# Optimization experiments

Measured on AMD Instinct MI355X. Metric: run time of the kernel, lower is better.

Reference implementation:

```python
import jax, jax.numpy as jnp
import numpy as np

DIM = 256
HEADS = 8
HEAD_DIM = DIM // HEADS
HIDDEN = DIM * 4


def layer_norm(x, w, b, eps=1e-5):
    m = jnp.mean(x, axis=-1, keepdims=True)
    v = jnp.mean((x - m) ** 2, axis=-1, keepdims=True)
    return (x - m) / jnp.sqrt(v + eps) * w + b


def setup_inputs() -> dict:
    key = jax.random.key(0)
    ks = jax.random.split(key, 12)
    s = lambda fan_in: 1.0 / np.sqrt(fan_in)
    inp = {
        "x0": jax.random.normal(ks[0], (2, 32, 64, DIM), jnp.float32),
        "x1": jax.random.normal(ks[1], (2, 32, 64, DIM), jnp.float32),
        # torch Linear weights stored [out, in], no bias for qk/v/merge
        "qk_w": jax.random.uniform(ks[2], (DIM, DIM), jnp.float32, -s(DIM), s(DIM)),
        "v_w": jax.random.uniform(ks[3], (DIM, DIM), jnp.float32, -s(DIM), s(DIM)),
        "merge_w": jax.random.uniform(ks[4], (DIM, DIM), jnp.float32, -s(DIM), s(DIM)),
        "ln1_w": jnp.ones((DIM,), jnp.float32),
        "ln1_b": jnp.zeros((DIM,), jnp.float32),
        "ln2_w": jnp.ones((DIM,), jnp.float32),
        "ln2_b": jnp.zeros((DIM,), jnp.float32),
        "fc1_w": jax.random.uniform(ks[5], (HIDDEN, 2 * DIM), jnp.float32, -s(2 * DIM), s(2 * DIM)),
        "fc1_b": jnp.zeros((HIDDEN,), jnp.float32),
        "fc2_w": jax.random.uniform(ks[6], (DIM, HIDDEN), jnp.float32, -s(HIDDEN), s(HIDDEN)),
        "fc2_b": jnp.zeros((DIM,), jnp.float32),
        "gamma": jnp.ones((DIM,), jnp.float32),
    }
    return inp


def reference(x0, x1, qk_w, v_w, merge_w, ln1_w, ln1_b, ln2_w, ln2_b,
              fc1_w, fc1_b, fc2_w, fc2_b, gamma):
    N0, L0, WW0, C = x0.shape
    N1, L1, WW1, _ = x1.shape
    x0f = x0.reshape(N0, L0 * WW0, C)
    x1f = x1.reshape(N1, L1 * WW1, C)

    n0 = layer_norm(x0f, ln1_w, ln1_b)
    n1 = layer_norm(x1f, ln1_w, ln1_b)

    def heads(t):  # [N, S, C] -> [N, H, S, Dh]
        N, S, _ = t.shape
        return t.reshape(N, S, HEADS, HEAD_DIM).transpose(0, 2, 1, 3)

    scale = HEAD_DIM ** -0.25  # sqrt of softmax_temp, applied to both sides
    qk0 = heads(n0 @ qk_w.T) * scale
    qk1 = heads(n1 @ qk_w.T) * scale
    v0 = heads(n0 @ v_w.T)
    v1 = heads(n1 @ v_w.T)

    # shared score matrix, reused for both softmax directions
    sim = jnp.einsum('bhld,bhsd->bhls', qk0, qk1)  # [N,H,L,S]
    attn01 = jax.nn.softmax(sim, axis=-1)
    attn10 = jax.nn.softmax(sim, axis=-2)  # == softmax(sim^T, -1)^T

    m0 = jnp.einsum('bhls,bhsd->bhld', attn01, v1)
    m1 = jnp.einsum('bhls,bhld->bhsd', attn10, v0)

    def unheads(t):  # [N,H,S,Dh] -> [N,S,C]
        N, H, S, D = t.shape
        return t.transpose(0, 2, 1, 3).reshape(N, S, H * D)

    m0 = unheads(m0) @ merge_w.T
    m1 = unheads(m1) @ merge_w.T

    def ffn_residual(x, m):
        h = jnp.concatenate([x, m], axis=-1)
        h = jax.nn.gelu(h @ fc1_w.T + fc1_b, approximate=False)
        h = h @ fc2_w.T + fc2_b
        return x + gamma * layer_norm(h, ln2_w, ln2_b)

    y0 = ffn_residual(x0f, m0).reshape(N0, L0, WW0, C)
    y1 = ffn_residual(x1f, m1).reshape(N1, L1, WW1, C)
    return (y0, y1)
```

## Files before the change

kernel.cpp:

```cpp
#include <hip/hip_runtime.h>
#include <hip/hip_bf16.h>
#include <math.h>


typedef float  f32x4  __attribute__((ext_vector_type(4)));
typedef __bf16 bf16x8 __attribute__((ext_vector_type(8)));

#define MFMA16(A, B, C) __builtin_amdgcn_mfma_f32_16x16x32_bf16((A), (B), (C), 0, 0, 0)

static constexpr int   ROWS  = 8192;
static constexpr float QK_SCALE = 0.42044820762685725f * 1.2011224087864498f;

__device__ inline unsigned short f2b(float f) {
    __hip_bfloat16 h = __float2bfloat16(f);
    union { __hip_bfloat16 h; unsigned short u; } cv;
    cv.h = h;
    return cv.u;
}

__device__ inline float exp2_fast(float x) {
    float r;
    asm("v_exp_f32 %0, %1\n\ts_nop 0" : "=v"(r) : "v"(x));
    return r;
}

__device__ inline float gelu_f(float x) {
    float z = 0.7978845608028654f * (x + 0.044715f * x * x * x);
    z = fminf(fmaxf(z, -15.0f), 15.0f);
    const float e = __expf(-2.0f * z);
    const float t = (1.0f - e) / (1.0f + e);
    return 0.5f * x * (1.0f + t);
}

__global__ __launch_bounds__(256) void cvt_w_kernel(
    const float* __restrict__ qkw, const float* __restrict__ vw,
    const float* __restrict__ mw,  const float* __restrict__ w1,
    const float* __restrict__ w2,  unsigned short* __restrict__ o)
{
    int i = blockIdx.x * 256 + threadIdx.x;
    float v;
    if      (i <  65536) v = qkw[i];
    else if (i < 131072) v = vw[i - 65536];
    else if (i < 196608) v = mw[i - 131072];
    else if (i < 720896) v = w1[i - 196608];
    else                 v = w2[i - 720896];
    o[i] = f2b(v);
}

__global__ __launch_bounds__(256) void ln_in_kernel(
    const float* __restrict__ x0, const float* __restrict__ x1,
    const float* __restrict__ w,  const float* __restrict__ b,
    unsigned short* __restrict__ nb,
    unsigned short* __restrict__ acat)
{
    const int wid  = threadIdx.x >> 6;
    const int lane = threadIdx.x & 63;
    const int row  = blockIdx.x * 4 + wid;
    const float* xr = (row < 4096) ? (x0 + (size_t)row * 256)
                                   : (x1 + (size_t)(row - 4096) * 256);
    const int c0 = lane * 4;
    const float4 xv = *(const float4*)(xr + c0);
    float s  = (xv.x + xv.y) + (xv.z + xv.w);
    float sq = (xv.x * xv.x + xv.y * xv.y) + (xv.z * xv.z + xv.w * xv.w);
#pragma unroll
    for (int off = 1; off < 64; off <<= 1) {
        s  += __shfl_xor(s,  off);
        sq += __shfl_xor(sq, off);
    }
    const float mean = s * (1.0f / 256.0f);
    const float var  = sq * (1.0f / 256.0f) - mean * mean;
    const float rs   = rsqrtf(var + 1e-5f);
    const float4 wv4 = *(const float4*)(w + c0);
    const float4 bv4 = *(const float4*)(b + c0);
    ushort4 nv;
    nv.x = f2b((xv.x - mean) * rs * wv4.x + bv4.x);
    nv.y = f2b((xv.y - mean) * rs * wv4.y + bv4.y);
    nv.z = f2b((xv.z - mean) * rs * wv4.z + bv4.z);
    nv.w = f2b((xv.w - mean) * rs * wv4.w + bv4.w);
    *(ushort4*)(nb + (size_t)row * 256 + c0) = nv;
    ushort4 xb;
    xb.x = f2b(xv.x); xb.y = f2b(xv.y); xb.z = f2b(xv.z); xb.w = f2b(xv.w);
    *(ushort4*)(acat + (size_t)row * 512 + c0) = xb;
}

__global__ __launch_bounds__(256) void gemm_qkv(
    const unsigned short* __restrict__ A, const unsigned short* __restrict__ W,
    unsigned short* __restrict__ qkb, unsigned short* __restrict__ vtb)
{
    constexpr int K = 256;
    __shared__ unsigned short As[64 * 72];
    __shared__ unsigned short Ws[64 * 72];
    const int tid  = threadIdx.x;
    const int wid  = tid >> 6;
    const int lane = tid & 63;
    const int ln   = lane & 15;
    const int quad = lane >> 4;
    const int m0 = blockIdx.x * 64, n0 = blockIdx.y * 64;
    f32x4 acc[4] = {{0,0,0,0},{0,0,0,0},{0,0,0,0},{0,0,0,0}};
    const int srow = tid >> 3;
    const int skc  = (tid & 7) * 8;
    const unsigned short* aP0 = A + (size_t)(m0 + srow)      * K + skc;
    const unsigned short* aP1 = A + (size_t)(m0 + srow + 32) * K + skc;
    const unsigned short* wP0 = W + (size_t)(n0 + srow)      * K + skc;
    const unsigned short* wP1 = W + (size_t)(n0 + srow + 32) * K + skc;
    for (int k0 = 0; k0 < K; k0 += 64) {
        *(uint4*)(As + srow * 72 + skc)        = *(const uint4*)(aP0 + k0);
        *(uint4*)(As + (srow + 32) * 72 + skc) = *(const uint4*)(aP1 + k0);
        *(uint4*)(Ws + srow * 72 + skc)        = *(const uint4*)(wP0 + k0);
        *(uint4*)(Ws + (srow + 32) * 72 + skc) = *(const uint4*)(wP1 + k0);
        __syncthreads();
#pragma unroll
        for (int kk = 0; kk < 64; kk += 32) {
            const bf16x8 af = *(const bf16x8*)(As + (wid * 16 + ln) * 72 + kk + quad * 8);
#pragma unroll
            for (int f = 0; f < 4; ++f) {
                const bf16x8 wf = *(const bf16x8*)(Ws + (f * 16 + ln) * 72 + kk + quad * 8);
                acc[f] = MFMA16(wf, af, acc[f]);
            }
        }
        __syncthreads();
    }
    const int rowm = m0 + wid * 16 + ln;
    if (n0 < 256) {
#pragma unroll
        for (int f = 0; f < 4; ++f) {
            const int cb = n0 + f * 16 + quad * 4;
            ushort4 o;
            o.x = f2b(acc[f][0] * QK_SCALE); o.y = f2b(acc[f][1] * QK_SCALE);
            o.z = f2b(acc[f][2] * QK_SCALE); o.w = f2b(acc[f][3] * QK_SCALE);
            *(ushort4*)(qkb + (size_t)rowm * 256 + cb) = o;
        }
    } else {
#pragma unroll
        for (int f = 0; f < 4; ++f) {
            const int cb = (n0 - 256) + f * 16 + quad * 4;
#pragma unroll
            for (int r = 0; r < 4; ++r)
                vtb[(size_t)(cb + r) * 8192 + rowm] = f2b(acc[f][r]);
        }
    }
}

__global__ __launch_bounds__(256) void gemm_merge(
    const unsigned short* __restrict__ A, const unsigned short* __restrict__ W,
    unsigned short* __restrict__ outB)
{
    constexpr int K = 256;
    __shared__ unsigned short As[64 * 72];
    __shared__ unsigned short Ws[64 * 72];
    const int tid  = threadIdx.x;
    const int wid  = tid >> 6;
    const int lane = tid & 63;
    const int ln   = lane & 15;
    const int quad = lane >> 4;
    const int m0 = blockIdx.x * 64, n0 = blockIdx.y * 64;
    f32x4 acc[4] = {{0,0,0,0},{0,0,0,0},{0,0,0,0},{0,0,0,0}};
    const int srow = tid >> 3;
    const int skc  = (tid & 7) * 8;
    const unsigned short* aP0 = A + (size_t)(m0 + srow)      * K + skc;
    const unsigned short* aP1 = A + (size_t)(m0 + srow + 32) * K + skc;
    const unsigned short* wP0 = W + (size_t)(n0 + srow)      * K + skc;
    const unsigned short* wP1 = W + (size_t)(n0 + srow + 32) * K + skc;
    for (int k0 = 0; k0 < K; k0 += 64) {
        *(uint4*)(As + srow * 72 + skc)        = *(const uint4*)(aP0 + k0);
        *(uint4*)(As + (srow + 32) * 72 + skc) = *(const uint4*)(aP1 + k0);
        *(uint4*)(Ws + srow * 72 + skc)        = *(const uint4*)(wP0 + k0);
        *(uint4*)(Ws + (srow + 32) * 72 + skc) = *(const uint4*)(wP1 + k0);
        __syncthreads();
#pragma unroll
        for (int kk = 0; kk < 64; kk += 32) {
            const bf16x8 af = *(const bf16x8*)(As + (wid * 16 + ln) * 72 + kk + quad * 8);
#pragma unroll
            for (int f = 0; f < 4; ++f) {
                const bf16x8 wf = *(const bf16x8*)(Ws + (f * 16 + ln) * 72 + kk + quad * 8);
                acc[f] = MFMA16(wf, af, acc[f]);
            }
        }
        __syncthreads();
    }
    const int rowm = m0 + wid * 16 + ln;
#pragma unroll
    for (int f = 0; f < 4; ++f) {
        const int cb = n0 + f * 16 + quad * 4;
        ushort4 o;
        o.x = f2b(acc[f][0]); o.y = f2b(acc[f][1]);
        o.z = f2b(acc[f][2]); o.w = f2b(acc[f][3]);
        *(ushort4*)(outB + (size_t)rowm * 512 + 256 + cb) = o;
    }
}

template <bool GELU_, bool OUTB>
__global__ __launch_bounds__(256) void gemm128(
    const unsigned short* __restrict__ A, const unsigned short* __restrict__ W,
    const float* __restrict__ bias,
    unsigned short* __restrict__ outB, float* __restrict__ outF,
    int K, int NS)
{
    __shared__ unsigned short As[128 * 72];
    __shared__ unsigned short Ws[128 * 72];
    const int tid  = threadIdx.x;
    const int wid  = tid >> 6;
    const int lane = tid & 63;
    const int ln   = lane & 15;
    const int quad = lane >> 4;
    const int m0 = blockIdx.x * 128, n0 = blockIdx.y * 128;
    const int wm = (wid & 1) * 64, wn = (wid >> 1) * 64;
    f32x4 acc[4][4];
#pragma unroll
    for (int f = 0; f < 4; ++f)
#pragma unroll
        for (int i = 0; i < 4; ++i) acc[f][i] = (f32x4){0, 0, 0, 0};
    const int sr = tid >> 2;
    const int sc = (tid & 3) * 8;
    for (int k0 = 0; k0 < K; k0 += 64) {
        const unsigned short* aB = A + (size_t)m0 * K + k0;
        const unsigned short* wB = W + (size_t)n0 * K + k0;
        *(uint4*)(As + sr * 72 + sc)             = *(const uint4*)(aB + (size_t)sr * K + sc);
        *(uint4*)(As + sr * 72 + sc + 32)        = *(const uint4*)(aB + (size_t)sr * K + sc + 32);
        *(uint4*)(As + (sr + 64) * 72 + sc)      = *(const uint4*)(aB + (size_t)(sr + 64) * K + sc);
        *(uint4*)(As + (sr + 64) * 72 + sc + 32) = *(const uint4*)(aB + (size_t)(sr + 64) * K + sc + 32);
        *(uint4*)(Ws + sr * 72 + sc)             = *(const uint4*)(wB + (size_t)sr * K + sc);
        *(uint4*)(Ws + sr * 72 + sc + 32)        = *(const uint4*)(wB + (size_t)sr * K + sc + 32);
        *(uint4*)(Ws + (sr + 64) * 72 + sc)      = *(const uint4*)(wB + (size_t)(sr + 64) * K + sc);
        *(uint4*)(Ws + (sr + 64) * 72 + sc + 32) = *(const uint4*)(wB + (size_t)(sr + 64) * K + sc + 32);
        __syncthreads();
#pragma unroll
        for (int kk = 0; kk < 64; kk += 32) {
            bf16x8 af[4], wf[4];
#pragma unroll
            for (int i = 0; i < 4; ++i)
                af[i] = *(const bf16x8*)(As + (wm + i * 16 + ln) * 72 + kk + quad * 8);
#pragma unroll
            for (int f = 0; f < 4; ++f)
                wf[f] = *(const bf16x8*)(Ws + (wn + f * 16 + ln) * 72 + kk + quad * 8);
#pragma unroll
            for (int f = 0; f < 4; ++f)
#pragma unroll
                for (int i = 0; i < 4; ++i)
                    acc[f][i] = MFMA16(wf[f], af[i], acc[f][i]);
        }
        __syncthreads();
    }
#pragma unroll
    for (int f = 0; f < 4; ++f) {
        const int feat = n0 + wn + f * 16 + quad * 4;
        const float4 b4 = *(const float4*)(bias + feat);
#pragma unroll
        for (int i = 0; i < 4; ++i) {
            const int token = m0 + wm + i * 16 + ln;
            float vv[4] = {acc[f][i][0] + b4.x, acc[f][i][1] + b4.y,
                           acc[f][i][2] + b4.z, acc[f][i][3] + b4.w};
            if (GELU_) {
#pragma unroll
                for (int r = 0; r < 4; ++r) vv[r] = gelu_f(vv[r]);
            }
            if (OUTB) {
                ushort4 o;
                o.x = f2b(vv[0]); o.y = f2b(vv[1]); o.z = f2b(vv[2]); o.w = f2b(vv[3]);
                *(ushort4*)(outB + (size_t)token * NS + feat) = o;
            } else {
                float4 o = {vv[0], vv[1], vv[2], vv[3]};
                *(float4*)(outF + (size_t)token * NS + feat) = o;
            }
        }
    }
}

__global__ __launch_bounds__(256, 4) void attn_kernel(
    const unsigned short* __restrict__ qk, const unsigned short* __restrict__ vtb,
    unsigned short* __restrict__ mo)
{
    __shared__ unsigned short Pw[4][64 * 40];
    const int tid  = threadIdx.x;
    const int wid  = tid >> 6;
    const int lane = tid & 63;
    const int ln   = lane & 15;
    const int quad = lane >> 4;
    const int dir = blockIdx.z, bh = blockIdx.y;
    const int b = bh >> 3, h = bh & 7;
    const int qbase = b * 2048 + (dir ? 4096 : 0);
    const int kbase = b * 2048 + (dir ? 0 : 4096);
    const int q0 = blockIdx.x * 64;
    const int xsw = (ln & 3) << 3;

    bf16x8 qf[4];
#pragma unroll
    for (int qg = 0; qg < 4; ++qg)
        qf[qg] = *(const bf16x8*)(qk + (size_t)(qbase + q0 + qg * 16 + ln) * 256 + h * 32 + quad * 8);

    f32x4 oacc[4][2];
#pragma unroll
    for (int qg = 0; qg < 4; ++qg) {
        oacc[qg][0] = (f32x4){0, 0, 0, 0};
        oacc[qg][1] = (f32x4){0, 0, 0, 0};
    }
    float lp[4] = {0.0f, 0.0f, 0.0f, 0.0f};
    const f32x4 zf = {0, 0, 0, 0};

    const unsigned short* kp = qk  + (size_t)(kbase + wid * 32 + ln) * 256 + h * 32 + quad * 8;
    const unsigned short* vp = vtb + (size_t)(h * 32 + ln) * 8192 + (kbase + wid * 32) + quad * 8;

    unsigned short* Pq[4];
#pragma unroll
    for (int qg = 0; qg < 4; ++qg) Pq[qg] = &Pw[wid][(qg * 16 + ln) * 40];

    bf16x8 kc0 = *(const bf16x8*)(kp);
    bf16x8 kc1 = *(const bf16x8*)(kp + 16 * 256);
    bf16x8 vc0 = *(const bf16x8*)(vp);
    bf16x8 vc1 = *(const bf16x8*)(vp + 16 * 8192);
    bf16x8 vn0, vn1;

    for (int it = 0; it < 16; ++it) {
#pragma unroll
        for (int sub = 0; sub < 2; ++sub) {
            const bf16x8 kf = sub ? kc1 : kc0;
            f32x4 s[4];
#pragma unroll
            for (int qg = 0; qg < 4; ++qg) s[qg] = MFMA16(kf, qf[qg], zf);
#pragma unroll
            for (int qg = 0; qg < 4; ++qg) {
                const float e0 = exp2_fast(s[qg][0]), e1 = exp2_fast(s[qg][1]);
                const float e2 = exp2_fast(s[qg][2]), e3 = exp2_fast(s[qg][3]);
                lp[qg] += (e0 + e1) + (e2 + e3);
                ushort4 pb;
                pb.x = f2b(e0); pb.y = f2b(e1); pb.z = f2b(e2); pb.w = f2b(e3);
                *(ushort4*)(Pq[qg] + ((sub * 16 + quad * 4) ^ xsw)) = pb;
            }
        }
        if (it < 15) {
            const unsigned short* kn = kp + (size_t)(it + 1) * 128 * 256;
            const unsigned short* vn = vp + (it + 1) * 128;
            kc0 = *(const bf16x8*)(kn);
            kc1 = *(const bf16x8*)(kn + 16 * 256);
            vn0 = *(const bf16x8*)(vn);
            vn1 = *(const bf16x8*)(vn + 16 * 8192);
        }
        asm volatile("s_waitcnt lgkmcnt(0)" ::: "memory");
#pragma unroll
        for (int qg = 0; qg < 4; ++qg) {
            const bf16x8 pf = *(const bf16x8*)(Pq[qg] + ((quad * 8) ^ xsw));
            oacc[qg][0] = MFMA16(vc0, pf, oacc[qg][0]);
            oacc[qg][1] = MFMA16(vc1, pf, oacc[qg][1]);
        }
        if (it < 15) { vc0 = vn0; vc1 = vn1; }
    }

#pragma unroll
    for (int qg = 0; qg < 4; ++qg) {
        lp[qg] += __shfl_xor(lp[qg], 16);
        lp[qg] += __shfl_xor(lp[qg], 32);
    }
    __syncthreads();
    float* scr  = (float*)&Pw[0][0];
    float* Lbuf = scr;
    float* Obuf = scr + 256;
    if (quad == 0) {
#pragma unroll
        for (int qg = 0; qg < 4; ++qg) Lbuf[wid * 64 + qg * 16 + ln] = lp[qg];
    }
#pragma unroll
    for (int qg = 0; qg < 4; ++qg) {
#pragma unroll
        for (int dg = 0; dg < 2; ++dg)
            *(f32x4*)&Obuf[(wid * 2 + dg) * 256 + lane * 4] = oacc[qg][dg];
        __syncthreads();
        if (wid == qg) {
            const int q = qg * 16 + ln;
            const float rinv = 1.0f /
                (Lbuf[q] + Lbuf[64 + q] + Lbuf[128 + q] + Lbuf[192 + q]);
            const size_t orow = (size_t)(qbase + q0 + q) * 256 + h * 32;
#pragma unroll
            for (int dg = 0; dg < 2; ++dg) {
                f32x4 sum = *(f32x4*)&Obuf[(0 + dg) * 256 + lane * 4];
#pragma unroll
                for (int w = 1; w < 4; ++w)
                    sum += *(f32x4*)&Obuf[(w * 2 + dg) * 256 + lane * 4];
                ushort4 o;
                o.x = f2b(sum[0] * rinv); o.y = f2b(sum[1] * rinv);
                o.z = f2b(sum[2] * rinv); o.w = f2b(sum[3] * rinv);
                *(ushort4*)(mo + orow + dg * 16 + quad * 4) = o;
            }
        }
        __syncthreads();
    }
}

__global__ __launch_bounds__(256) void ln_out_kernel(
    const float* __restrict__ x0, const float* __restrict__ x1,
    const float* __restrict__ h2, const float* __restrict__ w,
    const float* __restrict__ b,  const float* __restrict__ gamma,
    float* __restrict__ out)
{
    const int wid  = threadIdx.x >> 6;
    const int lane = threadIdx.x & 63;
    const int row  = blockIdx.x * 4 + wid;
    const int c0 = lane * 4;
    const float4 hv = *(const float4*)(h2 + (size_t)row * 256 + c0);
    float s  = (hv.x + hv.y) + (hv.z + hv.w);
    float sq = (hv.x * hv.x + hv.y * hv.y) + (hv.z * hv.z + hv.w * hv.w);
#pragma unroll
    for (int off = 1; off < 64; off <<= 1) {
        s  += __shfl_xor(s,  off);
        sq += __shfl_xor(sq, off);
    }
    const float mean = s * (1.0f / 256.0f);
    const float var  = sq * (1.0f / 256.0f) - mean * mean;
    const float rs   = rsqrtf(var + 1e-5f);
    const float* xr = (row < 4096) ? (x0 + (size_t)row * 256)
                                   : (x1 + (size_t)(row - 4096) * 256);
    const float4 xv = *(const float4*)(xr + c0);
    const float4 w4 = *(const float4*)(w + c0);
    const float4 b4 = *(const float4*)(b + c0);
    const float4 g4 = *(const float4*)(gamma + c0);
    float4 y;
    y.x = xv.x + g4.x * ((hv.x - mean) * rs * w4.x + b4.x);
    y.y = xv.y + g4.y * ((hv.y - mean) * rs * w4.y + b4.y);
    y.z = xv.z + g4.z * ((hv.z - mean) * rs * w4.z + b4.z);
    y.w = xv.w + g4.w * ((hv.w - mean) * rs * w4.w + b4.w);
    *(float4*)(out + (size_t)row * 256 + c0) = y;
}

extern "C" void kernel_launch(void* const* d_in, const int* in_sizes, int n_in,
                              void* d_out, int out_size, void* d_ws, size_t ws_size,
                              hipStream_t stream) {
    (void)in_sizes; (void)n_in; (void)out_size; (void)ws_size;
    const float* x0      = (const float*)d_in[0];
    const float* x1      = (const float*)d_in[1];
    const float* qk_w    = (const float*)d_in[2];
    const float* v_w     = (const float*)d_in[3];
    const float* merge_w = (const float*)d_in[4];
    const float* ln1_w   = (const float*)d_in[5];
    const float* ln1_b   = (const float*)d_in[6];
    const float* ln2_w   = (const float*)d_in[7];
    const float* ln2_b   = (const float*)d_in[8];
    const float* fc1_w   = (const float*)d_in[9];
    const float* fc1_b   = (const float*)d_in[10];
    const float* fc2_w   = (const float*)d_in[11];
    const float* fc2_b   = (const float*)d_in[12];
    const float* gamma   = (const float*)d_in[13];
    float* out = (float*)d_out;

    unsigned short* nb   = (unsigned short*)d_ws;
    unsigned short* qkb  = nb   + (size_t)ROWS * 256;
    unsigned short* vtb  = qkb  + (size_t)ROWS * 256;
    unsigned short* mb   = vtb  + (size_t)ROWS * 256;
    unsigned short* acat = mb   + (size_t)ROWS * 256;
    unsigned short* fc1o = acat + (size_t)ROWS * 512;
    float*          h2   = (float*)(fc1o + (size_t)ROWS * 1024);
    unsigned short* wqv  = (unsigned short*)(h2 + (size_t)ROWS * 256);
    unsigned short* wm   = wqv + 131072;
    unsigned short* w1   = wm  + 65536;
    unsigned short* w2   = w1  + 524288;

    cvt_w_kernel<<<3840, 256, 0, stream>>>(qk_w, v_w, merge_w, fc1_w, fc2_w, wqv);
    ln_in_kernel<<<2048, 256, 0, stream>>>(x0, x1, ln1_w, ln1_b, nb, acat);

    gemm_qkv<<<dim3(128, 8), 256, 0, stream>>>(nb, wqv, qkb, vtb);

    attn_kernel<<<dim3(32, 16, 2), 256, 0, stream>>>(qkb, vtb, mb);

    gemm_merge<<<dim3(128, 4), 256, 0, stream>>>(mb, wm, acat);

    gemm128<true, true><<<dim3(64, 8), 256, 0, stream>>>(
        acat, w1, fc1_b, fc1o, nullptr, 512, 1024);
    gemm128<false, false><<<dim3(64, 2), 256, 0, stream>>>(
        fc1o, w2, fc2_b, nullptr, h2, 1024, 256);

    ln_out_kernel<<<2048, 256, 0, stream>>>(x0, x1, h2, ln2_w, ln2_b, gamma, out);
}
```

Baseline: 186.5 us.

## Keep attention probabilities in registers by permuting V loads to match MFMA layout

The attention kernel no longer routes the exponentiated score tile through shared memory. V is loaded in a permuted key order (two 4-element chunks per lane), so the score MFMA output layout lines up directly with the B-operand of the PV MFMA. This removes the LDS write/read, the swizzle and the lgkmcnt wait. K is now double-buffered in registers, the loop is marked unroll 1, and exp2 moves from inline asm to a compiler builtin. The risks are narrower V loads, more register pressure and a shared-memory scratch layout that has changed.

```diff
diff --git a/kernel.cpp b/kernel.cpp
--- a/kernel.cpp
+++ b/kernel.cpp
@@ -19,9 +19,11 @@
 }
 
 __device__ inline float exp2_fast(float x) {
-    float r;
-    asm("v_exp_f32 %0, %1\n\ts_nop 0" : "=v"(r) : "v"(x));
-    return r;
+#if __has_builtin(__builtin_amdgcn_exp2f)
+    return __builtin_amdgcn_exp2f(x);
+#else
+    return __expf(x * 0.6931471805599453f);
+#endif
 }
 
 __device__ inline float gelu_f(float x) {
@@ -270,7 +272,7 @@
     const unsigned short* __restrict__ qk, const unsigned short* __restrict__ vtb,
     unsigned short* __restrict__ mo)
 {
-    __shared__ unsigned short Pw[4][64 * 40];
+    __shared__ float scr[2304];
     const int tid  = threadIdx.x;
     const int wid  = tid >> 6;
     const int lane = tid & 63;
@@ -281,7 +283,6 @@
     const int qbase = b * 2048 + (dir ? 4096 : 0);
     const int kbase = b * 2048 + (dir ? 0 : 4096);
     const int q0 = blockIdx.x * 64;
-    const int xsw = (ln & 3) << 3;
 
     bf16x8 qf[4];
 #pragma unroll
@@ -297,52 +298,56 @@
     float lp[4] = {0.0f, 0.0f, 0.0f, 0.0f};
     const f32x4 zf = {0, 0, 0, 0};
 
-    const unsigned short* kp = qk  + (size_t)(kbase + wid * 32 + ln) * 256 + h * 32 + quad * 8;
-    const unsigned short* vp = vtb + (size_t)(h * 32 + ln) * 8192 + (kbase + wid * 32) + quad * 8;
-
-    unsigned short* Pq[4];
-#pragma unroll
-    for (int qg = 0; qg < 4; ++qg) Pq[qg] = &Pw[wid][(qg * 16 + ln) * 40];
+    const int kb0 = kbase + wid * 32;
+    const unsigned short* kp  = qk  + (size_t)(kb0 + ln) * 256 + h * 32 + quad * 8;
+    const unsigned short* vp0 = vtb + (size_t)(h * 32 + ln)      * 8192 + kb0 + quad * 4;
+    const unsigned short* vp1 = vtb + (size_t)(h * 32 + 16 + ln) * 8192 + kb0 + quad * 4;
+
+    union bfu { ushort4 u2[2]; unsigned short u[8]; bf16x8 v; };
 
     bf16x8 kc0 = *(const bf16x8*)(kp);
     bf16x8 kc1 = *(const bf16x8*)(kp + 16 * 256);
-    bf16x8 vc0 = *(const bf16x8*)(vp);
-    bf16x8 vc1 = *(const bf16x8*)(vp + 16 * 8192);
-    bf16x8 vn0, vn1;
-
+    bfu vc0, vc1, vn0, vn1;
+    vc0.u2[0] = *(const ushort4*)(vp0);
+    vc0.u2[1] = *(const ushort4*)(vp0 + 16);
+    vc1.u2[0] = *(const ushort4*)(vp1);
+    vc1.u2[1] = *(const ushort4*)(vp1 + 16);
+
+#pragma unroll 1
     for (int it = 0; it < 16; ++it) {
-#pragma unroll
-        for (int sub = 0; sub < 2; ++sub) {
-            const bf16x8 kf = sub ? kc1 : kc0;
-            f32x4 s[4];
-#pragma unroll
-            for (int qg = 0; qg < 4; ++qg) s[qg] = MFMA16(kf, qf[qg], zf);
-#pragma unroll
-            for (int qg = 0; qg < 4; ++qg) {
-                const float e0 = exp2_fast(s[qg][0]), e1 = exp2_fast(s[qg][1]);
-                const float e2 = exp2_fast(s[qg][2]), e3 = exp2_fast(s[qg][3]);
-                lp[qg] += (e0 + e1) + (e2 + e3);
-                ushort4 pb;
-                pb.x = f2b(e0); pb.y = f2b(e1); pb.z = f2b(e2); pb.w = f2b(e3);
-                *(ushort4*)(Pq[qg] + ((sub * 16 + quad * 4) ^ xsw)) = pb;
-            }
-        }
+        bf16x8 kn0, kn1;
         if (it < 15) {
             const unsigned short* kn = kp + (size_t)(it + 1) * 128 * 256;
-            const unsigned short* vn = vp + (it + 1) * 128;
-            kc0 = *(const bf16x8*)(kn);
-            kc1 = *(const bf16x8*)(kn + 16 * 256);
-            vn0 = *(const bf16x8*)(vn);
-            vn1 = *(const bf16x8*)(vn + 16 * 8192);
-        }
-        asm volatile("s_waitcnt lgkmcnt(0)" ::: "memory");
+            kn0 = *(const bf16x8*)(kn);
+            kn1 = *(const bf16x8*)(kn + 16 * 256);
+            vn0.u2[0] = *(const ushort4*)(vp0 + (it + 1) * 128);
+            vn0.u2[1] = *(const ushort4*)(vp0 + (it + 1) * 128 + 16);
+            vn1.u2[0] = *(const ushort4*)(vp1 + (it + 1) * 128);
+            vn1.u2[1] = *(const ushort4*)(vp1 + (it + 1) * 128 + 16);
+        }
 #pragma unroll
         for (int qg = 0; qg < 4; ++qg) {
-            const bf16x8 pf = *(const bf16x8*)(Pq[qg] + ((quad * 8) ^ xsw));
-            oacc[qg][0] = MFMA16(vc0, pf, oacc[qg][0]);
-            oacc[qg][1] = MFMA16(vc1, pf, oacc[qg][1]);
-        }
-        if (it < 15) { vc0 = vn0; vc1 = vn1; }
+            const f32x4 s0 = MFMA16(kc0, qf[qg], zf);
+            const f32x4 s1 = MFMA16(kc1, qf[qg], zf);
+            bfu pf;
+            float es = 0.0f;
+#pragma unroll
+            for (int r = 0; r < 4; ++r) {
+                const float e = exp2_fast(s0[r]);
+                es += e;
+                pf.u[r] = f2b(e);
+            }
+#pragma unroll
+            for (int r = 0; r < 4; ++r) {
+                const float e = exp2_fast(s1[r]);
+                es += e;
+                pf.u[4 + r] = f2b(e);
+            }
+            lp[qg] += es;
+            oacc[qg][0] = MFMA16(vc0.v, pf.v, oacc[qg][0]);
+            oacc[qg][1] = MFMA16(vc1.v, pf.v, oacc[qg][1]);
+        }
+        if (it < 15) { kc0 = kn0; kc1 = kn1; vc0 = vn0; vc1 = vn1; }
     }
 
 #pragma unroll
@@ -350,8 +355,6 @@
         lp[qg] += __shfl_xor(lp[qg], 16);
         lp[qg] += __shfl_xor(lp[qg], 32);
     }
-    __syncthreads();
-    float* scr  = (float*)&Pw[0][0];
     float* Lbuf = scr;
     float* Obuf = scr + 256;
     if (quad == 0) {
```

New measurement: 222.0 us. 19.0% more time.
